# Optimization experiments

Hardware: AMD Instinct MI355X
Metric: run time of the kernel (lower is better)

## Reference

```python
import jax, jax.numpy as jnp
import numpy as np

LATENT_DIM = 64
EDGE_DIM = 4
HIDDEN_DIM = 32
N_NODES = 100000
N_EDGES = 1600000


def setup_inputs() -> dict:
    key = jax.random.key(0)
    ks = jax.random.split(key, 10)
    x = jax.random.normal(ks[0], (N_NODES, LATENT_DIM), dtype=jnp.float32)
    edge_index = jax.random.randint(ks[1], (2, N_EDGES), 0, N_NODES, dtype=jnp.int64)
    d2 = 2 * LATENT_DIM
    def lin(k, fan_in, fan_out):
        bound = 1.0 / np.sqrt(fan_in)
        kw, kb = jax.random.split(k)
        W = jax.random.uniform(kw, (fan_in, fan_out), jnp.float32, -bound, bound)
        b = jax.random.uniform(kb, (fan_out,), jnp.float32, -bound, bound)
        return W, b
    W_direct, b_direct = lin(ks[2], d2, EDGE_DIM)
    W1, b1 = lin(ks[3], d2, HIDDEN_DIM)
    W2, b2 = lin(ks[4], HIDDEN_DIM, HIDDEN_DIM)
    W3, b3 = lin(ks[5], HIDDEN_DIM, EDGE_DIM)
    return {
        "x": x, "edge_index": edge_index,
        "W_direct": W_direct, "b_direct": b_direct,
        "W1": W1, "b1": b1, "W2": W2, "b2": b2, "W3": W3, "b3": b3,
    }


def reference(x, edge_index, W_direct, b_direct, W1, b1, W2, b2, W3, b3):
    src, tgt = edge_index[0], edge_index[1]
    xs = x[src]  # [E, L] gather
    xt = x[tgt]  # [E, L] gather
    # elementwise min/max then concat -> [E, 2L]
    x_cat = jnp.concatenate([jnp.minimum(xs, xt), jnp.maximum(xs, xt)], axis=-1)
    h = jax.nn.relu(x_cat @ W1 + b1)           # [E, H]; dropout = identity (eval)
    h = jax.nn.relu((h @ W2 + b2) + h)         # residual block
    edge_pred = h @ W3 + b3                    # [E, edge_dim]
    pred_direct = x_cat @ W_direct + b_direct  # direct linear path
    return edge_pred + pred_direct
```

## Files before the change

kernel.cpp:

```cpp
#include <hip/hip_runtime.h>

typedef __attribute__((ext_vector_type(8))) short short8;
typedef __attribute__((ext_vector_type(4))) float f32x4;
typedef __attribute__((ext_vector_type(4))) unsigned int u32x4;

constexpr int HID = 32;
constexpr int LAT = 64;
constexpr int EPB = 256;
constexpr int NFRAG  = 12;
constexpr int NFRAG2 = 2;
constexpr int NFRAG3 = 1;

__device__ __forceinline__ unsigned pk2(float lo, float hi) {
    unsigned r;
    asm("v_cvt_pk_bf16_f32 %0, %1, %2" : "=v"(r) : "v"(lo), "v"(hi));
    return r;
}
__device__ __forceinline__ void mnmx_word(unsigned a, unsigned b, unsigned& mn, unsigned& mx) {
    float al = __uint_as_float(a << 16), ah = __uint_as_float(a & 0xFFFF0000u);
    float bl = __uint_as_float(b << 16), bh = __uint_as_float(b & 0xFFFF0000u);
    mn = pk2(fminf(al, bl), fminf(ah, bh));
    mx = pk2(fmaxf(al, bl), fmaxf(ah, bh));
}
struct MnMx4 { unsigned w0, w1, x0, x1; };
__device__ __forceinline__ MnMx4 mnmx4(float4 a, float4 b) {
    MnMx4 r;
    r.w0 = pk2(fminf(a.x, b.x), fminf(a.y, b.y));
    r.w1 = pk2(fminf(a.z, b.z), fminf(a.w, b.w));
    r.x0 = pk2(fmaxf(a.x, b.x), fmaxf(a.y, b.y));
    r.x1 = pk2(fmaxf(a.z, b.z), fmaxf(a.w, b.w));
    return r;
}

__global__ __launch_bounds__(256) void prep_kernel(const float* __restrict__ x,
                                                   const float* __restrict__ W1,
                                                   const float* __restrict__ Wd,
                                                   const float* __restrict__ W2,
                                                   const float* __restrict__ W3,
                                                   unsigned short* __restrict__ fr,
                                                   unsigned short* __restrict__ fr2,
                                                   unsigned short* __restrict__ fr3,
                                                   unsigned short* __restrict__ xb, int n8) {
    if (blockIdx.x < 4) {
        int id = blockIdx.x * 256 + threadIdx.x;
        if (id < NFRAG * 64) {
            int l = id & 63;
            int ft = id >> 6;
            int s = ft / 3, t = ft - s * 3;
            int g = l >> 4, c = l & 15;
            unsigned w[4];
            #pragma unroll
            for (int q = 0; q < 4; ++q) {
                int k = s * 32 + g * 8 + q * 2;
                float lo, hi;
                if (t < 2) { lo = W1[k * HID + t * 16 + c]; hi = W1[(k + 1) * HID + t * 16 + c]; }
                else { lo = (c < 4) ? Wd[k * 4 + c] : 0.0f; hi = (c < 4) ? Wd[(k + 1) * 4 + c] : 0.0f; }
                w[q] = pk2(lo, hi);
            }
            u32x4 v = { w[0], w[1], w[2], w[3] };
            ((u32x4*)fr)[ft * 64 + l] = v;
        } else if (id < (NFRAG + NFRAG2) * 64) {
            int f2 = id - NFRAG * 64;
            int l = f2 & 63;
            int t = f2 >> 6;
            int g = l >> 4, c = l & 15;
            int col = t * 16 + c;
            unsigned w[4];
            #pragma unroll
            for (int q = 0; q < 4; ++q) {
                int kb = (q < 2) ? (g * 4 + 2 * q) : (16 + g * 4 + 2 * (q - 2));
                float lo = W2[kb * HID + col] + (kb == col ? 1.0f : 0.0f);
                float hi = W2[(kb + 1) * HID + col] + ((kb + 1) == col ? 1.0f : 0.0f);
                w[q] = pk2(lo, hi);
            }
            u32x4 v = { w[0], w[1], w[2], w[3] };
            ((u32x4*)fr2)[t * 64 + l] = v;
        } else if (id < (NFRAG + NFRAG2 + NFRAG3) * 64) {
            int l = id - (NFRAG + NFRAG2) * 64;
            int g = l >> 4, c = l & 15;
            unsigned w[4];
            #pragma unroll
            for (int q = 0; q < 4; ++q) {
                int kb = (q < 2) ? (g * 4 + 2 * q) : (16 + g * 4 + 2 * (q - 2));
                float lo = (c < 4) ? W3[kb * 4 + c] : 0.0f;
                float hi = (c < 4) ? W3[(kb + 1) * 4 + c] : 0.0f;
                w[q] = pk2(lo, hi);
            }
            u32x4 v = { w[0], w[1], w[2], w[3] };
            ((u32x4*)fr3)[l] = v;
        }
    } else {
        int i = (blockIdx.x - 4) * 256 + threadIdx.x;
        if (i < n8) {
            const float4* p = (const float4*)x + (long)i * 2;
            float4 a = p[0], b = p[1];
            u32x4 v = { pk2(a.x, a.y), pk2(a.z, a.w), pk2(b.x, b.y), pk2(b.z, b.w) };
            ((u32x4*)xb)[i] = v;
        }
    }
}

template<int XMODE>
__global__ __launch_bounds__(256, 2) void edge_mfma_kernel(
    const float* __restrict__ xf,
    const unsigned short* __restrict__ xb,
    const unsigned short* __restrict__ fr,
    const unsigned short* __restrict__ fr2,
    const unsigned short* __restrict__ fr3,
    const int* __restrict__ ei,
    const float* __restrict__ b1, const float* __restrict__ bd,
    const float* __restrict__ b2, const float* __restrict__ b3,
    float* __restrict__ out, int E)
{
    const int tid = threadIdx.x;
    const int l = tid & 63;
    const int wv = tid >> 6;
    const int g = l >> 4, r = l & 15;
    const long waveBase = (long)blockIdx.x * EPB + wv * 64;

    short8 bfr[NFRAG];
    #pragma unroll
    for (int f = 0; f < NFRAG; ++f) bfr[f] = ((const short8*)fr)[f * 64 + l];
    short8 w2t[NFRAG2];
    #pragma unroll
    for (int f = 0; f < NFRAG2; ++f) w2t[f] = ((const short8*)fr2)[f * 64 + l];
    short8 w3t = ((const short8*)fr3)[l];

    const float4 b1a = ((const float4*)b1)[g], b1b = ((const float4*)b1)[4 + g];
    const float4 b2a = ((const float4*)b2)[g], b2b = ((const float4*)b2)[4 + g];
    f32x4 a2init;
    #pragma unroll
    for (int p = 0; p < 4; ++p) a2init[p] = (g == 0) ? (bd[p] + b3[p]) : 0.0f;

    int sidx[4], tidx[4];
    #pragma unroll
    for (int t = 0; t < 4; ++t) {
        long e = waveBase + t * 16 + r;
        long ecl = (e < E) ? e : (long)(E - 1);
        sidx[t] = ei[ecl];
        tidx[t] = ei[(long)E + ecl];
    }

    auto compute_tile = [&](short8 af0, short8 af1, short8 af2, short8 af3, int t) {
        f32x4 a0 = {0.f, 0.f, 0.f, 0.f}, a1 = a0;
        f32x4 a2 = a2init;
        a0 = __builtin_amdgcn_mfma_f32_16x16x32_bf16(bfr[0],  af0, a0, 0, 0, 0);
        a1 = __builtin_amdgcn_mfma_f32_16x16x32_bf16(bfr[1],  af0, a1, 0, 0, 0);
        a2 = __builtin_amdgcn_mfma_f32_16x16x32_bf16(bfr[2],  af0, a2, 0, 0, 0);
        a0 = __builtin_amdgcn_mfma_f32_16x16x32_bf16(bfr[3],  af1, a0, 0, 0, 0);
        a1 = __builtin_amdgcn_mfma_f32_16x16x32_bf16(bfr[4],  af1, a1, 0, 0, 0);
        a2 = __builtin_amdgcn_mfma_f32_16x16x32_bf16(bfr[5],  af1, a2, 0, 0, 0);
        a0 = __builtin_amdgcn_mfma_f32_16x16x32_bf16(bfr[6],  af2, a0, 0, 0, 0);
        a1 = __builtin_amdgcn_mfma_f32_16x16x32_bf16(bfr[7],  af2, a1, 0, 0, 0);
        a2 = __builtin_amdgcn_mfma_f32_16x16x32_bf16(bfr[8],  af2, a2, 0, 0, 0);
        a0 = __builtin_amdgcn_mfma_f32_16x16x32_bf16(bfr[9],  af3, a0, 0, 0, 0);
        a1 = __builtin_amdgcn_mfma_f32_16x16x32_bf16(bfr[10], af3, a1, 0, 0, 0);
        a2 = __builtin_amdgcn_mfma_f32_16x16x32_bf16(bfr[11], af3, a2, 0, 0, 0);

        union { short8 s; u32x4 u; } hf;
        hf.u[0] = pk2(fmaxf(a0[0] + b1a.x, 0.0f), fmaxf(a0[1] + b1a.y, 0.0f));
        hf.u[1] = pk2(fmaxf(a0[2] + b1a.z, 0.0f), fmaxf(a0[3] + b1a.w, 0.0f));
        hf.u[2] = pk2(fmaxf(a1[0] + b1b.x, 0.0f), fmaxf(a1[1] + b1b.y, 0.0f));
        hf.u[3] = pk2(fmaxf(a1[2] + b1b.z, 0.0f), fmaxf(a1[3] + b1b.w, 0.0f));

        f32x4 d0 = {0.f, 0.f, 0.f, 0.f}, d1 = d0;
        d0 = __builtin_amdgcn_mfma_f32_16x16x32_bf16(w2t[0], hf.s, d0, 0, 0, 0);
        d1 = __builtin_amdgcn_mfma_f32_16x16x32_bf16(w2t[1], hf.s, d1, 0, 0, 0);

        union { short8 s; u32x4 u; } hf2;
        hf2.u[0] = pk2(fmaxf(d0[0] + b2a.x, 0.0f), fmaxf(d0[1] + b2a.y, 0.0f));
        hf2.u[1] = pk2(fmaxf(d0[2] + b2a.z, 0.0f), fmaxf(d0[3] + b2a.w, 0.0f));
        hf2.u[2] = pk2(fmaxf(d1[0] + b2b.x, 0.0f), fmaxf(d1[1] + b2b.y, 0.0f));
        hf2.u[3] = pk2(fmaxf(d1[2] + b2b.z, 0.0f), fmaxf(d1[3] + b2b.w, 0.0f));

        f32x4 d3 = __builtin_amdgcn_mfma_f32_16x16x32_bf16(w3t, hf2.s, a2, 0, 0, 0);

        long e = waveBase + t * 16 + r;
        if (g == 0 && e < E)
            ((float4*)out)[e] = make_float4(d3[0], d3[1], d3[2], d3[3]);
    };

    if (XMODE == 1) {
        u32x4 Asl, Ash, Atl, Ath, Bsl, Bsh, Btl, Bth;
        #define GATHER(P, t) { \
            const u32x4* ps = (const u32x4*)(xb + (long)sidx[t] * LAT); \
            const u32x4* pt = (const u32x4*)(xb + (long)tidx[t] * LAT); \
            P##sl = ps[g]; P##sh = ps[4 + g]; P##tl = pt[g]; P##th = pt[4 + g]; }
        #define COMPUTE(P, t) { \
            union { short8 s; u32x4 u; } af0, af1, af2, af3; \
            _Pragma("unroll") \
            for (int q = 0; q < 4; ++q) { \
                unsigned mn, mx; \
                mnmx_word(P##sl[q], P##tl[q], mn, mx); af0.u[q] = mn; af2.u[q] = mx; \
                mnmx_word(P##sh[q], P##th[q], mn, mx); af1.u[q] = mn; af3.u[q] = mx; \
            } \
            compute_tile(af0.s, af1.s, af2.s, af3.s, t); }

        GATHER(A, 0)
        GATHER(B, 1)
        COMPUTE(A, 0)
        GATHER(A, 2)
        COMPUTE(B, 1)
        GATHER(B, 3)
        COMPUTE(A, 2)
        COMPUTE(B, 3)
        #undef GATHER
        #undef COMPUTE
    } else {
        #pragma unroll
        for (int t = 0; t < 4; ++t) {
            const float4* ps = (const float4*)(xf + (long)sidx[t] * LAT);
            const float4* pt = (const float4*)(xf + (long)tidx[t] * LAT);
            float4 sa = ps[2 * g], sb = ps[2 * g + 1], sc = ps[8 + 2 * g], sd = ps[9 + 2 * g];
            float4 ta = pt[2 * g], tb = pt[2 * g + 1], tc = pt[8 + 2 * g], td = pt[9 + 2 * g];
            MnMx4 m0 = mnmx4(sa, ta);
            MnMx4 m1 = mnmx4(sb, tb);
            MnMx4 m2 = mnmx4(sc, tc);
            MnMx4 m3 = mnmx4(sd, td);
            union { short8 s; u32x4 u; } af0, af1, af2, af3;
            af0.u[0] = m0.w0; af0.u[1] = m0.w1; af2.u[0] = m0.x0; af2.u[1] = m0.x1;
            af0.u[2] = m1.w0; af0.u[3] = m1.w1; af2.u[2] = m1.x0; af2.u[3] = m1.x1;
            af1.u[0] = m2.w0; af1.u[1] = m2.w1; af3.u[0] = m2.x0; af3.u[1] = m2.x1;
            af1.u[2] = m3.w0; af1.u[3] = m3.w1; af3.u[2] = m3.x0; af3.u[3] = m3.x1;
            compute_tile(af0.s, af1.s, af2.s, af3.s, t);
        }
    }
}

__global__ __launch_bounds__(256) void edge_pred_fp32_kernel(
    const float* __restrict__ x, const int* __restrict__ ei,
    const float* __restrict__ Wd, const float* __restrict__ bd,
    const float* __restrict__ W1, const float* __restrict__ b1,
    const float* __restrict__ W2, const float* __restrict__ b2,
    const float* __restrict__ W3, const float* __restrict__ b3,
    float* __restrict__ out, int E)
{
    int e = blockIdx.x * blockDim.x + threadIdx.x;
    if (e >= E) return;
    int s = ei[e];
    int t = ei[E + e];
    const float4* xs4 = (const float4*)(x + (long)s * 64);
    const float4* xt4 = (const float4*)(x + (long)t * 64);
    float h[HID];
    #pragma unroll
    for (int j = 0; j < HID; ++j) h[j] = b1[j];
    float d0 = bd[0], d1 = bd[1], d2 = bd[2], d3 = bd[3];
    #pragma unroll 2
    for (int c = 0; c < 16; ++c) {
        float4 a = xs4[c];
        float4 b = xt4[c];
        float mn[4] = {fminf(a.x,b.x), fminf(a.y,b.y), fminf(a.z,b.z), fminf(a.w,b.w)};
        float mx[4] = {fmaxf(a.x,b.x), fmaxf(a.y,b.y), fmaxf(a.z,b.z), fmaxf(a.w,b.w)};
        #pragma unroll
        for (int q = 0; q < 4; ++q) {
            int lidx = c * 4 + q;
            const float* wlo = W1 + lidx * HID;
            const float* whi = W1 + (64 + lidx) * HID;
            #pragma unroll
            for (int j = 0; j < HID; ++j) { h[j] += mn[q]*wlo[j]; h[j] += mx[q]*whi[j]; }
            const float* dlo = Wd + lidx * 4;
            const float* dhi = Wd + (64 + lidx) * 4;
            d0 += mn[q]*dlo[0] + mx[q]*dhi[0];
            d1 += mn[q]*dlo[1] + mx[q]*dhi[1];
            d2 += mn[q]*dlo[2] + mx[q]*dhi[2];
            d3 += mn[q]*dlo[3] + mx[q]*dhi[3];
        }
    }
    float h1[HID];
    #pragma unroll
    for (int j = 0; j < HID; ++j) h1[j] = fmaxf(h[j], 0.0f);
    float s2[HID];
    #pragma unroll
    for (int j = 0; j < HID; ++j) s2[j] = b2[j] + h1[j];
    #pragma unroll 4
    for (int k = 0; k < HID; ++k) {
        const float* w2r = W2 + k * HID;
        #pragma unroll
        for (int j = 0; j < HID; ++j) s2[j] += h1[k] * w2r[j];
    }
    float o0 = b3[0] + d0, o1 = b3[1] + d1, o2 = b3[2] + d2, o3 = b3[3] + d3;
    #pragma unroll
    for (int k = 0; k < HID; ++k) {
        float hk = fmaxf(s2[k], 0.0f);
        const float* w3r = W3 + k * 4;
        o0 += hk*w3r[0]; o1 += hk*w3r[1]; o2 += hk*w3r[2]; o3 += hk*w3r[3];
    }
    *(float4*)(out + (long)e * 4) = make_float4(o0, o1, o2, o3);
}

extern "C" void kernel_launch(void* const* d_in, const int* in_sizes, int n_in,
                              void* d_out, int out_size, void* d_ws, size_t ws_size,
                              hipStream_t stream) {
    const float* x  = (const float*)d_in[0];
    const int*   ei = (const int*)d_in[1];
    const float* Wd = (const float*)d_in[2];
    const float* bd = (const float*)d_in[3];
    const float* W1 = (const float*)d_in[4];
    const float* b1 = (const float*)d_in[5];
    const float* W2 = (const float*)d_in[6];
    const float* b2 = (const float*)d_in[7];
    const float* W3 = (const float*)d_in[8];
    const float* b3 = (const float*)d_in[9];
    float* out = (float*)d_out;

    int E  = in_sizes[1] / 2;
    int NN = in_sizes[0] / LAT;

    size_t fbytes  = (size_t)NFRAG  * 64 * 16;
    size_t f2bytes = (size_t)NFRAG2 * 64 * 16;
    size_t f3bytes = (size_t)NFRAG3 * 64 * 16;
    size_t fall    = fbytes + f2bytes + f3bytes;
    size_t fpad    = (fall + 255) & ~(size_t)255;
    size_t xbytes  = (size_t)NN * LAT * 2;

    int grid = (E + EPB - 1) / EPB;
    if (ws_size >= fpad + xbytes) {
        unsigned short* frg  = (unsigned short*)d_ws;
        unsigned short* frg2 = (unsigned short*)((char*)d_ws + fbytes);
        unsigned short* frg3 = (unsigned short*)((char*)d_ws + fbytes + f2bytes);
        unsigned short* xb   = (unsigned short*)((char*)d_ws + fpad);
        int n8 = NN * LAT / 8;
        int prep_grid = 4 + (n8 + 255) / 256;
        hipLaunchKernelGGL(prep_kernel, dim3(prep_grid), dim3(256), 0, stream,
                           x, W1, Wd, W2, W3, frg, frg2, frg3, xb, n8);
        hipLaunchKernelGGL((edge_mfma_kernel<1>), dim3(grid), dim3(256), 0, stream,
                           x, xb, frg, frg2, frg3, ei, b1, bd, b2, b3, out, E);
    } else if (ws_size >= fall) {
        unsigned short* frg  = (unsigned short*)d_ws;
        unsigned short* frg2 = (unsigned short*)((char*)d_ws + fbytes);
        unsigned short* frg3 = (unsigned short*)((char*)d_ws + fbytes + f2bytes);
        hipLaunchKernelGGL(prep_kernel, dim3(4), dim3(256), 0, stream,
                           x, W1, Wd, W2, W3, frg, frg2, frg3,
                           (unsigned short*)nullptr, 0);
        hipLaunchKernelGGL((edge_mfma_kernel<0>), dim3(grid), dim3(256), 0, stream,
                           x, (const unsigned short*)nullptr, frg, frg2, frg3,
                           ei, b1, bd, b2, b3, out, E);
    } else {
        hipLaunchKernelGGL(edge_pred_fp32_kernel, dim3((E + 255) / 256), dim3(256), 0, stream,
                           x, ei, Wd, bd, W1, b1, W2, b2, W3, b3, out, E);
    }
}
```

Baseline: 77.74 us.

## Make edge MFMA kernel persistent with cross-chunk gather and index prefetch

Converts the edge kernel to a grid-stride persistent loop capped at 1024 blocks. Each block loads its weight fragments once, then walks many 256-edge chunks, prefetching the next chunk's indices and starting its first row gathers while the current chunk is still being computed. Launch bounds rise from 2 to 4 blocks per CU to allow more waves in flight, at the cost of a tighter register budget that could force spills of the many register-held fragments.

Measured after the change: 112.6 us. 44.8% more time.

```diff
diff --git a/kernel.cpp b/kernel.cpp
--- a/kernel.cpp
+++ b/kernel.cpp
@@ -101,7 +101,7 @@
 }
 
 template<int XMODE>
-__global__ __launch_bounds__(256, 2) void edge_mfma_kernel(
+__global__ __launch_bounds__(256, 4) void edge_mfma_kernel(
     const float* __restrict__ xf,
     const unsigned short* __restrict__ xb,
     const unsigned short* __restrict__ fr,
@@ -110,13 +110,12 @@
     const int* __restrict__ ei,
     const float* __restrict__ b1, const float* __restrict__ bd,
     const float* __restrict__ b2, const float* __restrict__ b3,
-    float* __restrict__ out, int E)
+    float* __restrict__ out, int E, int nch)
 {
     const int tid = threadIdx.x;
     const int l = tid & 63;
     const int wv = tid >> 6;
     const int g = l >> 4, r = l & 15;
-    const long waveBase = (long)blockIdx.x * EPB + wv * 64;
 
     short8 bfr[NFRAG];
     #pragma unroll
@@ -132,16 +131,7 @@
     #pragma unroll
     for (int p = 0; p < 4; ++p) a2init[p] = (g == 0) ? (bd[p] + b3[p]) : 0.0f;
 
-    int sidx[4], tidx[4];
-    #pragma unroll
-    for (int t = 0; t < 4; ++t) {
-        long e = waveBase + t * 16 + r;
-        long ecl = (e < E) ? e : (long)(E - 1);
-        sidx[t] = ei[ecl];
-        tidx[t] = ei[(long)E + ecl];
-    }
-
-    auto compute_tile = [&](short8 af0, short8 af1, short8 af2, short8 af3, int t) {
+    auto compute_tile = [&](short8 af0, short8 af1, short8 af2, short8 af3, long estore) {
         f32x4 a0 = {0.f, 0.f, 0.f, 0.f}, a1 = a0;
         f32x4 a2 = a2init;
         a0 = __builtin_amdgcn_mfma_f32_16x16x32_bf16(bfr[0],  af0, a0, 0, 0, 0);
@@ -175,12 +165,25 @@
 
         f32x4 d3 = __builtin_amdgcn_mfma_f32_16x16x32_bf16(w3t, hf2.s, a2, 0, 0, 0);
 
-        long e = waveBase + t * 16 + r;
-        if (g == 0 && e < E)
-            ((float4*)out)[e] = make_float4(d3[0], d3[1], d3[2], d3[3]);
+        if (g == 0 && estore < E)
+            ((float4*)out)[estore] = make_float4(d3[0], d3[1], d3[2], d3[3]);
     };
 
+    int sidx[4], tidx[4], nsidx[4], ntidx[4];
+    auto load_idx = [&](int c, int* si, int* ti) {
+        long base = (long)c * EPB + wv * 64;
+        #pragma unroll
+        for (int t = 0; t < 4; ++t) {
+            long e = base + t * 16 + r;
+            long ecl = (e < E) ? e : (long)(E - 1);
+            si[t] = ei[ecl];
+            ti[t] = ei[(long)E + ecl];
+        }
+    };
+
     if (XMODE == 1) {
+        int c = blockIdx.x;
+        if (c >= nch) return;
         u32x4 Asl, Ash, Atl, Ath, Bsl, Bsh, Btl, Bth;
         #define GATHER(P, t) { \
             const u32x4* ps = (const u32x4*)(xb + (long)sidx[t] * LAT); \
@@ -194,35 +197,52 @@
                 mnmx_word(P##sl[q], P##tl[q], mn, mx); af0.u[q] = mn; af2.u[q] = mx; \
                 mnmx_word(P##sh[q], P##th[q], mn, mx); af1.u[q] = mn; af3.u[q] = mx; \
             } \
-            compute_tile(af0.s, af1.s, af2.s, af3.s, t); }
-
+            compute_tile(af0.s, af1.s, af2.s, af3.s, ebase + (t) * 16 + r); }
+
+        load_idx(c, sidx, tidx);
         GATHER(A, 0)
         GATHER(B, 1)
-        COMPUTE(A, 0)
-        GATHER(A, 2)
-        COMPUTE(B, 1)
-        GATHER(B, 3)
-        COMPUTE(A, 2)
-        COMPUTE(B, 3)
+        for (;;) {
+            const long ebase = (long)c * EPB + wv * 64;
+            const int cn = c + gridDim.x;
+            const bool more = (cn < nch);
+            COMPUTE(A, 0)
+            GATHER(A, 2)
+            COMPUTE(B, 1)
+            GATHER(B, 3)
+            if (more) load_idx(cn, nsidx, ntidx);
+            COMPUTE(A, 2)
+            COMPUTE(B, 3)
+            if (!more) break;
+            #pragma unroll
+            for (int t = 0; t < 4; ++t) { sidx[t] = nsidx[t]; tidx[t] = ntidx[t]; }
+            c = cn;
+            GATHER(A, 0)
+            GATHER(B, 1)
+        }
         #undef GATHER
         #undef COMPUTE
     } else {
-        #pragma unroll
-        for (int t = 0; t < 4; ++t) {
-            const float4* ps = (const float4*)(xf + (long)sidx[t] * LAT);
-            const float4* pt = (const float4*)(xf + (long)tidx[t] * LAT);
-            float4 sa = ps[2 * g], sb = ps[2 * g + 1], sc = ps[8 + 2 * g], sd = ps[9 + 2 * g];
-            float4 ta = pt[2 * g], tb = pt[2 * g + 1], tc = pt[8 + 2 * g], td = pt[9 + 2 * g];
-            MnMx4 m0 = mnmx4(sa, ta);
-            MnMx4 m1 = mnmx4(sb, tb);
-            MnMx4 m2 = mnmx4(sc, tc);
-            MnMx4 m3 = mnmx4(sd, td);
-            union { short8 s; u32x4 u; } af0, af1, af2, af3;
-            af0.u[0] = m0.w0; af0.u[1] = m0.w1; af2.u[0] = m0.x0; af2.u[1] = m0.x1;
-            af0.u[2] = m1.w0; af0.u[3] = m1.w1; af2.u[2] = m1.x0; af2.u[3] = m1.x1;
-            af1.u[0] = m2.w0; af1.u[1] = m2.w1; af3.u[0] = m2.x0; af3.u[1] = m2.x1;
-            af1.u[2] = m3.w0; af1.u[3] = m3.w1; af3.u[2] = m3.x0; af3.u[3] = m3.x1;
-            compute_tile(af0.s, af1.s, af2.s, af3.s, t);
+        for (int c = blockIdx.x; c < nch; c += gridDim.x) {
+            const long ebase = (long)c * EPB + wv * 64;
+            load_idx(c, sidx, tidx);
+            #pragma unroll
+            for (int t = 0; t < 4; ++t) {
+                const float4* ps = (const float4*)(xf + (long)sidx[t] * LAT);
+                const float4* pt = (const float4*)(xf + (long)tidx[t] * LAT);
+                float4 sa = ps[2 * g], sb = ps[2 * g + 1], sc = ps[8 + 2 * g], sd = ps[9 + 2 * g];
+                float4 ta = pt[2 * g], tb = pt[2 * g + 1], tc = pt[8 + 2 * g], td = pt[9 + 2 * g];
+                MnMx4 m0 = mnmx4(sa, ta);
+                MnMx4 m1 = mnmx4(sb, tb);
+                MnMx4 m2 = mnmx4(sc, tc);
+                MnMx4 m3 = mnmx4(sd, td);
+                union { short8 s; u32x4 u; } af0, af1, af2, af3;
+                af0.u[0] = m0.w0; af0.u[1] = m0.w1; af2.u[0] = m0.x0; af2.u[1] = m0.x1;
+                af0.u[2] = m1.w0; af0.u[3] = m1.w1; af2.u[2] = m1.x0; af2.u[3] = m1.x1;
+                af1.u[0] = m2.w0; af1.u[1] = m2.w1; af3.u[0] = m2.x0; af3.u[1] = m2.x1;
+                af1.u[2] = m3.w0; af1.u[3] = m3.w1; af3.u[2] = m3.x0; af3.u[3] = m3.x1;
+                compute_tile(af0.s, af1.s, af2.s, af3.s, ebase + t * 16 + r);
+            }
         }
     }
 }
@@ -305,6 +325,7 @@
 
     int E  = in_sizes[1] / 2;
     int NN = in_sizes[0] / LAT;
+    int nch = (E + EPB - 1) / EPB;
 
     size_t fbytes  = (size_t)NFRAG  * 64 * 16;
     size_t f2bytes = (size_t)NFRAG2 * 64 * 16;
@@ -313,7 +334,7 @@
     size_t fpad    = (fall + 255) & ~(size_t)255;
     size_t xbytes  = (size_t)NN * LAT * 2;
 
-    int grid = (E + EPB - 1) / EPB;
+    int grid = (nch < 1024) ? nch : 1024;
     if (ws_size >= fpad + xbytes) {
         unsigned short* frg  = (unsigned short*)d_ws;
         unsigned short* frg2 = (unsigned short*)((char*)d_ws + fbytes);
@@ -324,7 +345,7 @@
         hipLaunchKernelGGL(prep_kernel, dim3(prep_grid), dim3(256), 0, stream,
                            x, W1, Wd, W2, W3, frg, frg2, frg3, xb, n8);
         hipLaunchKernelGGL((edge_mfma_kernel<1>), dim3(grid), dim3(256), 0, stream,
-                           x, xb, frg, frg2, frg3, ei, b1, bd, b2, b3, out, E);
+                           x, xb, frg, frg2, frg3, ei, b1, bd, b2, b3, out, E, nch);
     } else if (ws_size >= fall) {
         unsigned short* frg  = (unsigned short*)d_ws;
         unsigned short* frg2 = (unsigned short*)((char*)d_ws + fbytes);
@@ -334,7 +355,7 @@
                            (unsigned short*)nullptr, 0);
         hipLaunchKernelGGL((edge_mfma_kernel<0>), dim3(grid), dim3(256), 0, stream,
                            x, (const unsigned short*)nullptr, frg, frg2, frg3,
-                           ei, b1, bd, b2, b3, out, E);
+                           ei, b1, bd, b2, b3, out, E, nch);
     } else {
         hipLaunchKernelGGL(edge_pred_fp32_kernel, dim3((E + 255) / 256), dim3(256), 0, stream,
                            x, ei, Wd, bd, W1, b1, W2, b2, W3, b3, out, E);
```
